# Kernel optimization log

Measured on AMD Instinct MI355X. Metric: run time of the kernel, lower is better.

## Reference

```python
import jax, jax.numpy as jnp
import numpy as np

N = 50000      # nodes
E = 800000     # edges (before self-loops)
F_IN = 128     # args.nsegment
H = 4          # args.nhead
C = 32         # args.dhidden
OUT = 64       # output_dim
G = 64         # number of graphs in batch
NEG = 0.2      # args.negslope (and GATv2 internal leaky-relu slope, PyG default 0.2)


def setup_inputs() -> dict:
    key = jax.random.key(0)
    ks = jax.random.split(key, 8)
    def w(k, i, o):
        return jax.random.normal(k, (i, o), jnp.float32) / np.sqrt(i)
    x = jax.random.normal(ks[0], (N, F_IN), jnp.float32)
    edge_index = jax.random.randint(ks[1], (2, E), 0, N, dtype=jnp.int32)
    batch = jnp.sort(jax.random.randint(ks[2], (N,), 0, G, dtype=jnp.int32))
    d = dict(x=x, edge_index=edge_index, batch=batch)
    # layer dims: (in_dim, heads, out_per_head, concat)
    dims = [(F_IN, H, C, True), (H * C, H, C, True), (H * C, 1, OUT, False)]
    for li, (fi, h, c, concat) in enumerate(dims):
        k1, k2, k3 = jax.random.split(ks[3 + li], 3)
        d[f"Wl{li}"] = w(k1, fi, h * c)
        d[f"Wr{li}"] = w(k2, fi, h * c)
        d[f"att{li}"] = jax.random.normal(k3, (h, c), jnp.float32) / np.sqrt(c)
        d[f"b{li}"] = jnp.zeros((h * c if concat else c,), jnp.float32)
    return d


def _gat_layer(x, src, tgt, Wl, Wr, att, b, concat):
    """GATv2Conv: e_ij = att . leaky_relu(Wl x_j + Wr x_i); softmax over edges into i;
    out_i = sum_j alpha_ij * (Wl x_j). src/tgt include self-loops."""
    n = x.shape[0]
    h, c = att.shape
    xl = (x @ Wl).reshape(n, h, c)                 # source transform [N,h,c]
    xr = (x @ Wr).reshape(n, h, c)                 # target transform [N,h,c]
    g = jax.nn.leaky_relu(xl[src] + xr[tgt], NEG)  # [Etot,h,c]
    score = jnp.einsum('ehc,hc->eh', g, att)       # [Etot,h]
    smax = jax.ops.segment_max(score, tgt, num_segments=n)
    ex = jnp.exp(score - smax[tgt])
    den = jax.ops.segment_sum(ex, tgt, num_segments=n)
    alpha = ex / den[tgt]                          # per-target softmax [Etot,h]
    out = jax.ops.segment_sum(xl[src] * alpha[:, :, None], tgt, num_segments=n)
    out = out.reshape(n, h * c) if concat else out.mean(axis=1)
    return out + b


def _forward(x, edge_index, batch, params):
    n = x.shape[0]
    loops = jnp.arange(n, dtype=edge_index.dtype)  # PyG add_self_loops=True
    src = jnp.concatenate([edge_index[0], loops])
    tgt = jnp.concatenate([edge_index[1], loops])
    for Wl, Wr, att, b, concat in params:
        x = _gat_layer(x, src, tgt, Wl, Wr, att, b, concat)
        x = jax.nn.leaky_relu(x, NEG)  # dropout p is identity in eval mode
    ssum = jax.ops.segment_sum(x, batch, num_segments=G)
    cnt = jax.ops.segment_sum(jnp.ones((n,), x.dtype), batch, num_segments=G)
    return ssum / jnp.maximum(cnt, 1.0)[:, None]   # global_mean_pool -> [G, OUT]


def reference(x, edge_index, batch, Wl0, Wr0, att0, b0, Wl1, Wr1, att1, b1, Wl2, Wr2, att2, b2):
    params = [(Wl0, Wr0, att0, b0, True),
              (Wl1, Wr1, att1, b1, True),
              (Wl2, Wr2, att2, b2, False)]
    return _forward(x, edge_index, batch, params)
```

## Files before the change

### kernel.cpp

```cpp
#include <hip/hip_runtime.h>
#include <hip/hip_fp16.h>
#include <math.h>

#define NEGSLOPE 0.2f

typedef _Float16 f16x8 __attribute__((ext_vector_type(8)));
typedef float f32x4 __attribute__((ext_vector_type(4)));

__device__ __forceinline__ float lrelu(float x) { return x > 0.f ? x : NEGSLOPE * x; }

__global__ __launch_bounds__(256) void k_prep(
        const float* __restrict__ x, _Float16* __restrict__ xh, int n8, int XB,
        const float* W0, const float* W1, const float* W2,
        const float* W3, const float* W4, const float* W5,
        _Float16* D0, _Float16* D1, _Float16* D2,
        _Float16* D3, _Float16* D4, _Float16* D5,
        int* __restrict__ deg, float* __restrict__ pacc, int n, int npacc) {
    int b = blockIdx.x, t = threadIdx.x;
    if (b < XB) {
        int i = b * 256 + t;
        if (i < n8) {
            float4 a = ((const float4*)x)[2 * i], c = ((const float4*)x)[2 * i + 1];
            union { uint4 u; _Float16 h[8]; } pk;
            pk.h[0] = (_Float16)a.x; pk.h[1] = (_Float16)a.y;
            pk.h[2] = (_Float16)a.z; pk.h[3] = (_Float16)a.w;
            pk.h[4] = (_Float16)c.x; pk.h[5] = (_Float16)c.y;
            pk.h[6] = (_Float16)c.z; pk.h[7] = (_Float16)c.w;
            ((uint4*)xh)[i] = pk.u;
        }
    } else if (b < XB + 320) {
        const float* Ws[6] = {W0, W1, W2, W3, W4, W5};
        _Float16* Ds[6] = {D0, D1, D2, D3, D4, D5};
        int j = (b - XB) * 256 + t;
        int m, jj, kout;
        if (j < 65536) { m = j >> 14; jj = j & 16383; kout = 128; }
        else           { m = 4 + ((j - 65536) >> 13); jj = (j - 65536) & 8191; kout = 64; }
        int col = jj >> 7, k = jj & 127;
        Ds[m][col * 128 + k] = (_Float16)Ws[m][k * kout + col];
    } else {
        int i = (b - XB - 320) * 256 + t;
        if (i < n) deg[i] = 0;
        else if (i < n + npacc) pacc[i - n] = 0.f;
    }
}

__global__ void k_count(const int* __restrict__ tgt, int* __restrict__ deg,
                        int* __restrict__ rank, int e) {
    int i = blockIdx.x * 256 + threadIdx.x;
    if (i < e) rank[i] = atomicAdd(&deg[tgt[i]], 1);
}
__global__ __launch_bounds__(256) void k_scanA(const int* __restrict__ deg, int* __restrict__ rowptr,
                                               int* __restrict__ bsums, int n) {
    __shared__ int s[256];
    int t = threadIdx.x;
    int base = blockIdx.x * 4096 + t * 16;
    int pre[16];
    int sum = 0;
    for (int i = 0; i < 16; ++i) {
        int idx = base + i;
        int v = (idx < n) ? (deg[idx] + 1) : 0;
        pre[i] = sum;
        sum += v;
    }
    s[t] = sum;
    __syncthreads();
    for (int off = 1; off < 256; off <<= 1) {
        int v = (t >= off) ? s[t - off] : 0;
        __syncthreads();
        s[t] += v;
        __syncthreads();
    }
    int tbase = s[t] - sum;
    for (int i = 0; i < 16; ++i) {
        int idx = base + i;
        if (idx < n) rowptr[idx] = tbase + pre[i];
    }
    if (t == 0) bsums[blockIdx.x] = s[255];
}
__global__ __launch_bounds__(256) void k_scanC(int* __restrict__ rowptr, const int* __restrict__ bsums,
                                               int* __restrict__ edst, int nscan, int n) {
    __shared__ int pref[65];
    int t = threadIdx.x;
    if (t == 0) {
        int run = 0;
        for (int k = 0; k < nscan; ++k) { pref[k] = run; run += bsums[k]; }
        pref[nscan] = run;
    }
    __syncthreads();
    int i = blockIdx.x * 256 + t;
    if (i < n) {
        int rp = rowptr[i] + pref[i >> 12];
        rowptr[i] = rp;
        edst[rp] = i;
    }
    if (blockIdx.x == gridDim.x - 1 && t == 0) rowptr[n] = pref[nscan];
}
__global__ void k_scatter(const int* __restrict__ src, const int* __restrict__ tgt,
                          const int* __restrict__ rank, const int* __restrict__ rowptr,
                          int* __restrict__ edst, int e) {
    int i = blockIdx.x * 256 + threadIdx.x;
    if (i < e) {
        int p = rowptr[tgt[i]] + 1 + rank[i];
        __builtin_nontemporal_store(src[i], &edst[p]);
    }
}

template<int KOUT>
__global__ __launch_bounds__(256) void k_gemm_mfma(
        const _Float16* __restrict__ Ah,
        const _Float16* __restrict__ Wt0, const _Float16* __restrict__ Wt1,
        _Float16* __restrict__ out0, _Float16* __restrict__ out1, int n) {
    int wv = threadIdx.x >> 6, lane = threadIdx.x & 63;
    int m = lane & 15, q = lane >> 4;
    int row0 = blockIdx.x * 64 + wv * 16;
    int arow = row0 + m; if (arow >= n) arow = n - 1;
    const _Float16* ap = Ah + (size_t)arow * 128 + q * 8;
    f16x8 af[4];
#pragma unroll
    for (int kt = 0; kt < 4; ++kt) af[kt] = *(const f16x8*)(ap + 32 * kt);

    const _Float16* Wp = Wt0;
    _Float16* outp = out0;
    if (KOUT == 128 && blockIdx.y) { Wp = Wt1; outp = out1; }

    f32x4 acc[8] = {};
#pragma unroll
    for (int kt = 0; kt < 4; ++kt) {
        f16x8 bfr[8];
#pragma unroll
        for (int ct = 0; ct < 8; ++ct) {
            const _Float16* W = (KOUT == 128) ? Wp : (ct < 4 ? Wt0 : Wt1);
            int col0 = (KOUT == 128) ? ct * 16 : (ct & 3) * 16;
            bfr[ct] = *(const f16x8*)(W + (size_t)(col0 + m) * 128 + 32 * kt + 8 * q);
        }
#pragma unroll
        for (int ct = 0; ct < 8; ++ct)
            acc[ct] = __builtin_amdgcn_mfma_f32_16x16x32_f16(af[kt], bfr[ct], acc[ct], 0, 0, 0);
    }
#pragma unroll
    for (int ct = 0; ct < 8; ++ct) {
        _Float16* dst = (KOUT == 128) ? outp : (ct < 4 ? out0 : out1);
        int col = ((KOUT == 128) ? ct * 16 : (ct & 3) * 16) + m;
#pragma unroll
        for (int i = 0; i < 4; ++i) {
            int r = row0 + q * 4 + i;
            if (r < n) dst[(size_t)r * KOUT + col] = (_Float16)acc[ct][i];
        }
    }
}

template<int H, int C, typename OutT>
__global__ __launch_bounds__(256) void k_agg(const __half* __restrict__ xl, const __half* __restrict__ xr,
                                             const float* __restrict__ att, const float* __restrict__ bias,
                                             const int* __restrict__ rowptr, const int* __restrict__ edst,
                                             OutT* __restrict__ yout, int n) {
    constexpr int F = H * C;
    constexpr int VEC = F / 16;
    constexpr int L = C / VEC;
    int lane = threadIdx.x & 63;
    int wave = threadIdx.x >> 6;
    int s = lane & 15;
    int node = blockIdx.x * 16 + wave * 4 + (lane >> 4);
    bool valid = node < n;
    int nodeSafe = valid ? node : 0;
    int ch = s * VEC;

    auto loadrow = [&](const __half* base, int row, float* v) {
        const __half* p = base + (size_t)row * F + ch;
        if constexpr (VEC == 8) {
            union { uint4 u4; __half2 h[4]; } pk;
            pk.u4 = *(const uint4*)p;
#pragma unroll
            for (int j = 0; j < 4; ++j) {
                float2 f = __half22float2(pk.h[j]);
                v[2 * j] = f.x; v[2 * j + 1] = f.y;
            }
        } else {
            union { uint2 u2; __half2 h[2]; } pk;
            pk.u2 = *(const uint2*)p;
#pragma unroll
            for (int j = 0; j < 2; ++j) {
                float2 f = __half22float2(pk.h[j]);
                v[2 * j] = f.x; v[2 * j + 1] = f.y;
            }
        }
    };

    float u[VEC], av[VEC], acc[VEC];
    loadrow(xr, nodeSafe, u);
#pragma unroll
    for (int j = 0; j < VEC; ++j) {
        av[j] = att[ch + j];
        acc[j] = 0.f;
    }
    int e0 = rowptr[nodeSafe];
    int deg = valid ? (rowptr[nodeSafe + 1] - e0) : 0;
    int maxdeg = deg;
    maxdeg = max(maxdeg, __shfl_xor(maxdeg, 16));
    maxdeg = max(maxdeg, __shfl_xor(maxdeg, 32));
    float ssum = 0.f;

    auto dot = [&](const float* v) {
        float p = 0.f;
#pragma unroll
        for (int j = 0; j < VEC; ++j) p += lrelu(v[j] + u[j]) * av[j];
        return p;
    };
    auto accum = [&](float w, const float* v) {
        ssum += w;
#pragma unroll
        for (int j = 0; j < VEC; ++j) acc[j] += w * v[j];
    };

    for (int base = 0; base < maxdeg; base += 16) {
        int cnt = deg - base;
        if (cnt > 16) cnt = 16;
        int idxreg = (s < cnt) ? edst[e0 + base + s] : nodeSafe;
        int mcnt = cnt;
        mcnt = max(mcnt, __shfl_xor(mcnt, 16));
        mcnt = max(mcnt, __shfl_xor(mcnt, 32));
        int gbase = lane & 48;
        int i = 0;
        for (; i + 4 <= mcnt; i += 4) {
            int s0 = __shfl(idxreg, gbase + i);
            int s1 = __shfl(idxreg, gbase + i + 1);
            int s2 = __shfl(idxreg, gbase + i + 2);
            int s3 = __shfl(idxreg, gbase + i + 3);
            float v0[VEC], v1[VEC], v2[VEC], v3[VEC];
            loadrow(xl, s0, v0); loadrow(xl, s1, v1);
            loadrow(xl, s2, v2); loadrow(xl, s3, v3);
            float p0 = dot(v0), p1 = dot(v1), p2 = dot(v2), p3 = dot(v3);
#pragma unroll
            for (int off = 1; off < L; off <<= 1) {
                p0 += __shfl_xor(p0, off);
                p1 += __shfl_xor(p1, off);
                p2 += __shfl_xor(p2, off);
                p3 += __shfl_xor(p3, off);
            }
            float w0 = (i + 0 < cnt) ? __expf(p0) : 0.f;
            float w1 = (i + 1 < cnt) ? __expf(p1) : 0.f;
            float w2 = (i + 2 < cnt) ? __expf(p2) : 0.f;
            float w3 = (i + 3 < cnt) ? __expf(p3) : 0.f;
            accum(w0, v0); accum(w1, v1); accum(w2, v2); accum(w3, v3);
        }
        for (; i < mcnt; ++i) {
            int s0 = __shfl(idxreg, gbase + i);
            float v[VEC];
            loadrow(xl, s0, v);
            float p = dot(v);
#pragma unroll
            for (int off = 1; off < L; off <<= 1) p += __shfl_xor(p, off);
            float w = (i < cnt) ? __expf(p) : 0.f;
            accum(w, v);
        }
    }
    if (valid) {
        float inv = 1.f / ssum;
        float o[VEC];
#pragma unroll
        for (int j = 0; j < VEC; ++j) o[j] = lrelu(acc[j] * inv + bias[ch + j]);
        if constexpr (sizeof(OutT) == 2) {
            _Float16* p = (_Float16*)yout + (size_t)node * F + ch;
            if constexpr (VEC == 8) {
                union { uint4 u; _Float16 h[8]; } pk;
#pragma unroll
                for (int j = 0; j < 8; ++j) pk.h[j] = (_Float16)o[j];
                *(uint4*)p = pk.u;
            } else {
                union { uint2 u; _Float16 h[4]; } pk;
#pragma unroll
                for (int j = 0; j < 4; ++j) pk.h[j] = (_Float16)o[j];
                *(uint2*)p = pk.u;
            }
        } else {
            float* p = (float*)yout + (size_t)node * F + ch;
            *(float4*)p = make_float4(o[0], o[1], o[2], o[3]);
            if constexpr (VEC == 8)
                *(float4*)(p + 4) = make_float4(o[4], o[5], o[6], o[7]);
        }
    }
}

__global__ __launch_bounds__(256) void k_pool_partial(const float* __restrict__ y,
        const int* __restrict__ batch, float* __restrict__ pacc, int n, int nchunk) {
    __shared__ float sdata[256];
    __shared__ int range[2];
    int g = blockIdx.x;
    int chunk = blockIdx.y;
    int t = threadIdx.x;
    if (t == 0) {
        int lo = 0, hi = n;
        while (lo < hi) { int mid = (lo + hi) >> 1; if (batch[mid] < g) lo = mid + 1; else hi = mid; }
        range[0] = lo;
        hi = n;
        while (lo < hi) { int mid = (lo + hi) >> 1; if (batch[mid] < g + 1) lo = mid + 1; else hi = mid; }
        range[1] = lo;
    }
    __syncthreads();
    int start = range[0], len = range[1] - range[0];
    int lo = start + (int)((long long)len * chunk / nchunk);
    int hi = start + (int)((long long)len * (chunk + 1) / nchunk);
    int ch = t & 63, sub = t >> 6;
    float acc = 0.f;
    for (int node = lo + sub; node < hi; node += 4)
        acc += y[(size_t)node * 64 + ch];
    sdata[t] = acc;
    __syncthreads();
    if (t < 128) sdata[t] += sdata[t + 128];
    __syncthreads();
    if (t < 64) atomicAdd(&pacc[g * 64 + t], sdata[t] + sdata[t + 64]);
}
__global__ void k_pool_final(const float* __restrict__ pacc, const int* __restrict__ batch,
                             float* __restrict__ out, int n) {
    __shared__ int cntS;
    int g = blockIdx.x, t = threadIdx.x;
    if (t == 0) {
        int lo = 0, hi = n;
        while (lo < hi) { int mid = (lo + hi) >> 1; if (batch[mid] < g) lo = mid + 1; else hi = mid; }
        int s = lo;
        hi = n;
        while (lo < hi) { int mid = (lo + hi) >> 1; if (batch[mid] < g + 1) lo = mid + 1; else hi = mid; }
        cntS = lo - s;
    }
    __syncthreads();
    out[g * 64 + t] = pacc[g * 64 + t] / fmaxf((float)cntS, 1.f);
}

extern "C" void kernel_launch(void* const* d_in, const int* in_sizes, int n_in,
                              void* d_out, int out_size, void* d_ws, size_t ws_size,
                              hipStream_t stream) {
    const float* x     = (const float*)d_in[0];
    const int*   ei    = (const int*)d_in[1];
    const int*   batch = (const int*)d_in[2];
    const float* Wl0 = (const float*)d_in[3];
    const float* Wr0 = (const float*)d_in[4];
    const float* att0 = (const float*)d_in[5];
    const float* b0  = (const float*)d_in[6];
    const float* Wl1 = (const float*)d_in[7];
    const float* Wr1 = (const float*)d_in[8];
    const float* att1 = (const float*)d_in[9];
    const float* b1  = (const float*)d_in[10];
    const float* Wl2 = (const float*)d_in[11];
    const float* Wr2 = (const float*)d_in[12];
    const float* att2 = (const float*)d_in[13];
    const float* b2  = (const float*)d_in[14];

    const int N = in_sizes[2];
    const int E = in_sizes[1] / 2;
    const int G = out_size / 64;
    const int* src = ei;
    const int* tgt = ei + E;

    size_t off = 0;
    auto take = [&](size_t bytes) {
        void* p = (char*)d_ws + off;
        off = (off + bytes + 255) & ~(size_t)255;
        return p;
    };
    _Float16* xh   = (_Float16*)take((size_t)N * 128 * 2);
    _Float16* Ah   = (_Float16*)take((size_t)N * 128 * 2);
    _Float16* B    = (_Float16*)take((size_t)N * 128 * 2);
    _Float16* Cbh  = (_Float16*)take((size_t)N * 128 * 2);
    float* Cbf     = (float*)take((size_t)N * 64 * 4);
    _Float16* Wl0t = (_Float16*)take(128 * 128 * 2);
    _Float16* Wr0t = (_Float16*)take(128 * 128 * 2);
    _Float16* Wl1t = (_Float16*)take(128 * 128 * 2);
    _Float16* Wr1t = (_Float16*)take(128 * 128 * 2);
    _Float16* Wl2t = (_Float16*)take(64 * 128 * 2);
    _Float16* Wr2t = (_Float16*)take(64 * 128 * 2);
    int* rowptr = (int*)take((size_t)(N + 1) * 4);
    int* tmp    = (int*)take((size_t)N * 4);
    float* pacc = (float*)take((size_t)G * 64 * 4);
    int* rank   = (int*)take((size_t)E * 4);
    int* edst   = (int*)take((size_t)(E + N) * 4);
    int* bsums  = (int*)take(64 * 4);
    (void)ws_size; (void)n_in;

    const int TB = 256;
    int nblkN = (N + TB - 1) / TB;
    int nblkE = (E + TB - 1) / TB;
    int nscan = (N + 4095) / 4096;

    int n8 = N * 128 / 8;
    int XB = (n8 + TB - 1) / TB;
    int ZB = (N + G * 64 + TB - 1) / TB;
    k_prep<<<XB + 320 + ZB, TB, 0, stream>>>(x, xh, n8, XB,
        Wl0, Wr0, Wl1, Wr1, Wl2, Wr2,
        Wl0t, Wr0t, Wl1t, Wr1t, Wl2t, Wr2t,
        tmp, pacc, N, G * 64);

    k_count<<<nblkE, TB, 0, stream>>>(tgt, tmp, rank, E);
    k_scanA<<<nscan, TB, 0, stream>>>(tmp, rowptr, bsums, N);
    k_scanC<<<nblkN, TB, 0, stream>>>(rowptr, bsums, edst, nscan, N);
    k_scatter<<<nblkE, TB, 0, stream>>>(src, tgt, rank, rowptr, edst, E);

    int gemmBlocks = (N + 63) / 64;
    dim3 gemmGrid2(gemmBlocks, 2);
    dim3 gemmGrid1(gemmBlocks, 1);
    int aggBlocks = (N + 15) / 16;

    k_gemm_mfma<128><<<gemmGrid2, TB, 0, stream>>>(xh, Wl0t, Wr0t, Ah, B, N);
    k_agg<4, 32, _Float16><<<aggBlocks, TB, 0, stream>>>((const __half*)Ah, (const __half*)B, att0, b0, rowptr, edst, Cbh, N);

    k_gemm_mfma<128><<<gemmGrid2, TB, 0, stream>>>(Cbh, Wl1t, Wr1t, Ah, B, N);
    k_agg<4, 32, _Float16><<<aggBlocks, TB, 0, stream>>>((const __half*)Ah, (const __half*)B, att1, b1, rowptr, edst, Cbh, N);

    k_gemm_mfma<64><<<gemmGrid1, TB, 0, stream>>>(Cbh, Wl2t, Wr2t, Ah, B, N);
    k_agg<1, 64, float><<<aggBlocks, TB, 0, stream>>>((const __half*)Ah, (const __half*)B, att2, b2, rowptr, edst, Cbf, N);

    dim3 poolGrid(G, 16);
    k_pool_partial<<<poolGrid, TB, 0, stream>>>(Cbf, batch, pacc, N, 16);
    k_pool_final<<<G, 64, 0, stream>>>(pacc, batch, (float*)d_out, N);
}
```

Measured before the change: 380.6 us.

## Sort aggregation nodes by degree and compute attention scores with packed fp16 dot2

Builds a degree histogram during the scan and uses it to write a degree-bucketed node permutation. Each aggregation wave then handles four nodes of similar degree, which cuts the idle lanes caused by the per-wave max-degree loop. The attention score is now computed in packed fp16 math (add, leaky-relu via max, fdot2) instead of converting to fp32 first, and the per-edge unroll drops from 4 to 2. The cost is an extra tiny kernel, atomics during the scan, lower score precision, and less sequential locality in node order.

```diff
diff --git a/kernel.cpp b/kernel.cpp
--- a/kernel.cpp
+++ b/kernel.cpp
@@ -5,9 +5,18 @@
 #define NEGSLOPE 0.2f
 
 typedef _Float16 f16x8 __attribute__((ext_vector_type(8)));
+typedef _Float16 f16x2 __attribute__((ext_vector_type(2)));
 typedef float f32x4 __attribute__((ext_vector_type(4)));
 
 __device__ __forceinline__ float lrelu(float x) { return x > 0.f ? x : NEGSLOPE * x; }
+
+__device__ __forceinline__ float dot2acc(f16x2 a, f16x2 b, float c) {
+#if __has_builtin(__builtin_amdgcn_fdot2)
+    return __builtin_amdgcn_fdot2(a, b, c, false);
+#else
+    return c + (float)a[0] * (float)b[0] + (float)a[1] * (float)b[1];
+#endif
+}
 
 __global__ __launch_bounds__(256) void k_prep(
         const float* __restrict__ x, _Float16* __restrict__ xh, int n8, int XB,
@@ -15,7 +24,7 @@
         const float* W3, const float* W4, const float* W5,
         _Float16* D0, _Float16* D1, _Float16* D2,
         _Float16* D3, _Float16* D4, _Float16* D5,
-        int* __restrict__ deg, float* __restrict__ pacc, int n, int npacc) {
+        int* __restrict__ zbase, int nzero) {
     int b = blockIdx.x, t = threadIdx.x;
     if (b < XB) {
         int i = b * 256 + t;
@@ -39,8 +48,7 @@
         Ds[m][col * 128 + k] = (_Float16)Ws[m][k * kout + col];
     } else {
         int i = (b - XB - 320) * 256 + t;
-        if (i < n) deg[i] = 0;
-        else if (i < n + npacc) pacc[i - n] = 0.f;
+        if (i < nzero) zbase[i] = 0;
     }
 }
 
@@ -50,15 +58,22 @@
     if (i < e) rank[i] = atomicAdd(&deg[tgt[i]], 1);
 }
 __global__ __launch_bounds__(256) void k_scanA(const int* __restrict__ deg, int* __restrict__ rowptr,
-                                               int* __restrict__ bsums, int n) {
+                                               int* __restrict__ bsums, int* __restrict__ ghist, int n) {
     __shared__ int s[256];
+    __shared__ int lh[64];
     int t = threadIdx.x;
+    if (t < 64) lh[t] = 0;
     int base = blockIdx.x * 4096 + t * 16;
     int pre[16];
     int sum = 0;
+    __syncthreads();
     for (int i = 0; i < 16; ++i) {
         int idx = base + i;
-        int v = (idx < n) ? (deg[idx] + 1) : 0;
+        int v = 0;
+        if (idx < n) {
+            v = deg[idx] + 1;
+            atomicAdd(&lh[v < 63 ? v : 63], 1);
+        }
         pre[i] = sum;
         sum += v;
     }
@@ -76,9 +91,18 @@
         if (idx < n) rowptr[idx] = tbase + pre[i];
     }
     if (t == 0) bsums[blockIdx.x] = s[255];
+    if (t < 64 && lh[t]) atomicAdd(&ghist[t], lh[t]);
+}
+__global__ void k_binit(const int* __restrict__ ghist, int* __restrict__ cursor) {
+    if (threadIdx.x == 0) {
+        int run = 0;
+        for (int b = 0; b < 64; ++b) { cursor[b] = run; run += ghist[b]; }
+    }
 }
 __global__ __launch_bounds__(256) void k_scanC(int* __restrict__ rowptr, const int* __restrict__ bsums,
-                                               int* __restrict__ edst, int nscan, int n) {
+                                               int* __restrict__ edst, const int* __restrict__ deg,
+                                               int* __restrict__ cursor, int* __restrict__ perm,
+                                               int nscan, int n) {
     __shared__ int pref[65];
     int t = threadIdx.x;
     if (t == 0) {
@@ -92,6 +116,9 @@
         int rp = rowptr[i] + pref[i >> 12];
         rowptr[i] = rp;
         edst[rp] = i;
+        int d = deg[i] + 1;
+        int p = atomicAdd(&cursor[d < 63 ? d : 63], 1);
+        perm[p] = i;
     }
     if (blockIdx.x == gridDim.x - 1 && t == 0) rowptr[n] = pref[nscan];
 }
@@ -150,108 +177,89 @@
 }
 
 template<int H, int C, typename OutT>
-__global__ __launch_bounds__(256) void k_agg(const __half* __restrict__ xl, const __half* __restrict__ xr,
+__global__ __launch_bounds__(256) void k_agg(const _Float16* __restrict__ xl, const _Float16* __restrict__ xr,
                                              const float* __restrict__ att, const float* __restrict__ bias,
                                              const int* __restrict__ rowptr, const int* __restrict__ edst,
+                                             const int* __restrict__ perm,
                                              OutT* __restrict__ yout, int n) {
     constexpr int F = H * C;
     constexpr int VEC = F / 16;
+    constexpr int NH2 = VEC / 2;
     constexpr int L = C / VEC;
     int lane = threadIdx.x & 63;
     int wave = threadIdx.x >> 6;
     int s = lane & 15;
-    int node = blockIdx.x * 16 + wave * 4 + (lane >> 4);
-    bool valid = node < n;
-    int nodeSafe = valid ? node : 0;
+    int gid = blockIdx.x * 16 + wave * 4 + (lane >> 4);
+    bool valid = gid < n;
+    int node = valid ? perm[gid] : 0;
     int ch = s * VEC;
 
-    auto loadrow = [&](const __half* base, int row, float* v) {
-        const __half* p = base + (size_t)row * F + ch;
-        if constexpr (VEC == 8) {
-            union { uint4 u4; __half2 h[4]; } pk;
-            pk.u4 = *(const uint4*)p;
-#pragma unroll
-            for (int j = 0; j < 4; ++j) {
-                float2 f = __half22float2(pk.h[j]);
-                v[2 * j] = f.x; v[2 * j + 1] = f.y;
-            }
-        } else {
-            union { uint2 u2; __half2 h[2]; } pk;
-            pk.u2 = *(const uint2*)p;
-#pragma unroll
-            for (int j = 0; j < 2; ++j) {
-                float2 f = __half22float2(pk.h[j]);
-                v[2 * j] = f.x; v[2 * j + 1] = f.y;
-            }
-        }
-    };
-
-    float u[VEC], av[VEC], acc[VEC];
-    loadrow(xr, nodeSafe, u);
-#pragma unroll
-    for (int j = 0; j < VEC; ++j) {
-        av[j] = att[ch + j];
-        acc[j] = 0.f;
-    }
-    int e0 = rowptr[nodeSafe];
-    int deg = valid ? (rowptr[nodeSafe + 1] - e0) : 0;
+    f16x2 u2[NH2], av2[NH2];
+    {
+        union { uint4 u4; uint2 u2v; f16x2 h[4]; } pk;
+        if constexpr (NH2 == 4) pk.u4 = *(const uint4*)(xr + (size_t)node * F + ch);
+        else pk.u2v = *(const uint2*)(xr + (size_t)node * F + ch);
+#pragma unroll
+        for (int j = 0; j < NH2; ++j) u2[j] = pk.h[j];
+    }
+#pragma unroll
+    for (int j = 0; j < NH2; ++j) {
+        av2[j][0] = (_Float16)att[ch + 2 * j];
+        av2[j][1] = (_Float16)att[ch + 2 * j + 1];
+    }
+
+    float acc[VEC];
+#pragma unroll
+    for (int j = 0; j < VEC; ++j) acc[j] = 0.f;
+    int e0 = rowptr[node];
+    int deg = valid ? (rowptr[node + 1] - e0) : 0;
     int maxdeg = deg;
     maxdeg = max(maxdeg, __shfl_xor(maxdeg, 16));
     maxdeg = max(maxdeg, __shfl_xor(maxdeg, 32));
     float ssum = 0.f;
 
-    auto dot = [&](const float* v) {
-        float p = 0.f;
-#pragma unroll
-        for (int j = 0; j < VEC; ++j) p += lrelu(v[j] + u[j]) * av[j];
-        return p;
-    };
-    auto accum = [&](float w, const float* v) {
+    const _Float16 cneg = (_Float16)NEGSLOPE;
+    auto edge = [&](int srcRow, bool live) {
+        union { uint4 u4; uint2 u2v; f16x2 hh[4]; } pk;
+        const _Float16* p = xl + (size_t)srcRow * F + ch;
+        if constexpr (NH2 == 4) pk.u4 = *(const uint4*)p;
+        else pk.u2v = *(const uint2*)p;
+        float sc = 0.f;
+#pragma unroll
+        for (int j = 0; j < NH2; ++j) {
+            f16x2 t = pk.hh[j] + u2[j];
+            f16x2 lr = __builtin_elementwise_max(t, t * cneg);
+            sc = dot2acc(lr, av2[j], sc);
+        }
+#pragma unroll
+        for (int off = 1; off < L; off <<= 1) sc += __shfl_xor(sc, off);
+        float w = live ? __expf(sc) : 0.f;
         ssum += w;
 #pragma unroll
-        for (int j = 0; j < VEC; ++j) acc[j] += w * v[j];
+        for (int j = 0; j < NH2; ++j) {
+            acc[2 * j]     += w * (float)pk.hh[j][0];
+            acc[2 * j + 1] += w * (float)pk.hh[j][1];
+        }
     };
 
     for (int base = 0; base < maxdeg; base += 16) {
         int cnt = deg - base;
         if (cnt > 16) cnt = 16;
-        int idxreg = (s < cnt) ? edst[e0 + base + s] : nodeSafe;
+        int idxreg = (s < cnt) ? edst[e0 + base + s] : node;
         int mcnt = cnt;
         mcnt = max(mcnt, __shfl_xor(mcnt, 16));
         mcnt = max(mcnt, __shfl_xor(mcnt, 32));
         int gbase = lane & 48;
         int i = 0;
-        for (; i + 4 <= mcnt; i += 4) {
+        for (; i + 2 <= mcnt; i += 2) {
             int s0 = __shfl(idxreg, gbase + i);
             int s1 = __shfl(idxreg, gbase + i + 1);
-            int s2 = __shfl(idxreg, gbase + i + 2);
-            int s3 = __shfl(idxreg, gbase + i + 3);
-            float v0[VEC], v1[VEC], v2[VEC], v3[VEC];
-            loadrow(xl, s0, v0); loadrow(xl, s1, v1);
-            loadrow(xl, s2, v2); loadrow(xl, s3, v3);
-            float p0 = dot(v0), p1 = dot(v1), p2 = dot(v2), p3 = dot(v3);
-#pragma unroll
-            for (int off = 1; off < L; off <<= 1) {
-                p0 += __shfl_xor(p0, off);
-                p1 += __shfl_xor(p1, off);
-                p2 += __shfl_xor(p2, off);
-                p3 += __shfl_xor(p3, off);
-            }
-            float w0 = (i + 0 < cnt) ? __expf(p0) : 0.f;
-            float w1 = (i + 1 < cnt) ? __expf(p1) : 0.f;
-            float w2 = (i + 2 < cnt) ? __expf(p2) : 0.f;
-            float w3 = (i + 3 < cnt) ? __expf(p3) : 0.f;
-            accum(w0, v0); accum(w1, v1); accum(w2, v2); accum(w3, v3);
+            edge(s0, i < cnt);
+            edge(s1, i + 1 < cnt);
         }
         for (; i < mcnt; ++i) {
             int s0 = __shfl(idxreg, gbase + i);
-            float v[VEC];
-            loadrow(xl, s0, v);
-            float p = dot(v);
-#pragma unroll
-            for (int off = 1; off < L; off <<= 1) p += __shfl_xor(p, off);
-            float w = (i < cnt) ? __expf(p) : 0.f;
-            accum(w, v);
+            edge(s0, i < cnt);
         }
     }
     if (valid) {
@@ -371,6 +379,9 @@
     int* rowptr = (int*)take((size_t)(N + 1) * 4);
     int* tmp    = (int*)take((size_t)N * 4);
     float* pacc = (float*)take((size_t)G * 64 * 4);
+    int* ghist  = (int*)take(64 * 4);
+    int* cursor = (int*)take(64 * 4);
+    int* perm   = (int*)take((size_t)N * 4);
     int* rank   = (int*)take((size_t)E * 4);
     int* edst   = (int*)take((size_t)(E + N) * 4);
     int* bsums  = (int*)take(64 * 4);
@@ -383,15 +394,17 @@
 
     int n8 = N * 128 / 8;
     int XB = (n8 + TB - 1) / TB;
-    int ZB = (N + G * 64 + TB - 1) / TB;
+    int nzero = (int)(((char*)(cursor)) - (char*)tmp) / 4;
+    int ZB = (nzero + TB - 1) / TB;
     k_prep<<<XB + 320 + ZB, TB, 0, stream>>>(x, xh, n8, XB,
         Wl0, Wr0, Wl1, Wr1, Wl2, Wr2,
         Wl0t, Wr0t, Wl1t, Wr1t, Wl2t, Wr2t,
-        tmp, pacc, N, G * 64);
+        tmp, nzero);
 
     k_count<<<nblkE, TB, 0, stream>>>(tgt, tmp, rank, E);
-    k_scanA<<<nscan, TB, 0, stream>>>(tmp, rowptr, bsums, N);
-    k_scanC<<<nblkN, TB, 0, stream>>>(rowptr, bsums, edst, nscan, N);
+    k_scanA<<<nscan, TB, 0, stream>>>(tmp, rowptr, bsums, ghist, N);
+    k_binit<<<1, 64, 0, stream>>>(ghist, cursor);
+    k_scanC<<<nblkN, TB, 0, stream>>>(rowptr, bsums, edst, tmp, cursor, perm, nscan, N);
     k_scatter<<<nblkE, TB, 0, stream>>>(src, tgt, rank, rowptr, edst, E);
 
     int gemmBlocks = (N + 63) / 64;
@@ -400,13 +413,13 @@
     int aggBlocks = (N + 15) / 16;
 
     k_gemm_mfma<128><<<gemmGrid2, TB, 0, stream>>>(xh, Wl0t, Wr0t, Ah, B, N);
-    k_agg<4, 32, _Float16><<<aggBlocks, TB, 0, stream>>>((const __half*)Ah, (const __half*)B, att0, b0, rowptr, edst, Cbh, N);
+    k_agg<4, 32, _Float16><<<aggBlocks, TB, 0, stream>>>(Ah, B, att0, b0, rowptr, edst, perm, Cbh, N);
 
     k_gemm_mfma<128><<<gemmGrid2, TB, 0, stream>>>(Cbh, Wl1t, Wr1t, Ah, B, N);
-    k_agg<4, 32, _Float16><<<aggBlocks, TB, 0, stream>>>((const __half*)Ah, (const __half*)B, att1, b1, rowptr, edst, Cbh, N);
+    k_agg<4, 32, _Float16><<<aggBlocks, TB, 0, stream>>>(Ah, B, att1, b1, rowptr, edst, perm, Cbh, N);
 
     k_gemm_mfma<64><<<gemmGrid1, TB, 0, stream>>>(Cbh, Wl2t, Wr2t, Ah, B, N);
-    k_agg<1, 64, float><<<aggBlocks, TB, 0, stream>>>((const __half*)Ah, (const __half*)B, att2, b2, rowptr, edst, Cbf, N);
+    k_agg<1, 64, float><<<aggBlocks, TB, 0, stream>>>(Ah, B, att2, b2, rowptr, edst, perm, Cbf, N);
 
     dim3 poolGrid(G, 16);
     k_pool_partial<<<poolGrid, TB, 0, stream>>>(Cbf, batch, pacc, N, 16);
```

Result: slower. 503.2 us (+32.2%).
